# Kernel tuning notes

Hardware: AMD Instinct MI355X
Metric: run time of the kernel (lower is better)

Reference implementation:

```python
import jax, jax.numpy as jnp
import numpy as np


def setup_inputs() -> dict:
    key = jax.random.key(0)
    ks = jax.random.split(key, 6)
    B, C, H, W, O = 8, 64, 64, 64, 64
    x = jax.random.normal(ks[0], (B, C, H, W), jnp.float32)
    wq = jax.random.normal(ks[1], (O, C), jnp.float32) * 0.1
    wk = jax.random.normal(ks[2], (O, C), jnp.float32) * 0.1
    wv = jax.random.normal(ks[3], (O, C), jnp.float32) * 0.1
    rel_w = jax.random.normal(ks[4], (O, W), jnp.float32)
    rel_h = jax.random.normal(ks[5], (O, H), jnp.float32)
    return {"x": x, "wq": wq, "wk": wk, "wv": wv,
            "rel_w": rel_w, "rel_h": rel_h,
            "kernel_size": 7, "padding": 3}


def reference(x, wq, wk, wv, rel_w, rel_h, kernel_size, padding):
    B, C, H, W = x.shape
    k, p = kernel_size, padding
    # 1x1 convs (no bias) == channel matmuls
    q = jnp.einsum('bchw,oc->bohw', x, wq)                      # [B,O,H,W]
    xp = jnp.pad(x, ((0, 0), (0, 0), (p, p), (p, p)))
    k_out = jnp.einsum('bchw,oc->bohw', xp, wk)                 # [B,O,H+2p,W+2p]
    v_out = jnp.einsum('bchw,oc->bohw', xp, wv)

    def patches(t):  # torch unfold(2).unfold(3) order: row offset slowest
        return jnp.stack([t[:, :, i:i + H, j:j + W]
                          for i in range(k) for j in range(k)], axis=-1)  # [B,O,H,W,k*k]

    kp = patches(k_out)
    vp = patches(v_out)
    # relative position logits (broadcast elementwise einsums)
    rel = q * rel_w[None, :, None, :] + q * rel_h[None, :, :, None]  # [B,O,H,W]
    logits = q[..., None] * kp + rel[..., None]                 # [B,O,H,W,k*k]
    attn = jax.nn.softmax(logits, axis=-1)
    return jnp.sum(attn * vp, axis=-1)                          # [B,O,H,W]
```

## Files before the change

### kernel.cpp

```cpp
#include <hip/hip_runtime.h>
#include <hip/hip_bf16.h>

#define HW 4096

__device__ float g_qkv[3 * 8 * 64 * HW];

__global__ __launch_bounds__(256) void qkv_proj(
    const float* __restrict__ x,
    const float* __restrict__ wq,
    const float* __restrict__ wk,
    const float* __restrict__ wv)
{
    __shared__ float xs[64][64];
    const int t = threadIdx.x;
    const int b = blockIdx.x >> 6;
    const int h = blockIdx.x & 63;

    const float* xrow = x + (size_t)b * 64 * HW + (size_t)h * 64;
    for (int i = t; i < 64 * 64; i += 256) {
        int c = i >> 6, w = i & 63;
        xs[c][w] = xrow[(size_t)c * HW + w];
    }
    __syncthreads();

    const int w = t & 63;
    const int ou = __builtin_amdgcn_readfirstlane(t >> 6);

    float xr[64];
    #pragma unroll
    for (int c = 0; c < 64; ++c) xr[c] = xs[c][w];

    const float* __restrict__ mats[3] = { wq, wk, wv };
    #pragma unroll
    for (int m = 0; m < 3; ++m) {
        const float* __restrict__ wg = mats[m];
        float* op = g_qkv + ((size_t)m * 8 + b) * (64 * HW) + (size_t)h * 64 + w;
        #pragma unroll
        for (int oi = 0; oi < 16; ++oi) {
            const int o = oi * 4 + ou;
            const float* __restrict__ wrow = wg + (o << 6);
            float acc = 0.f;
            #pragma unroll
            for (int c = 0; c < 64; ++c)
                acc = fmaf(wrow[c], xr[c], acc);
            op[(size_t)o * HW] = acc;
        }
    }
}

__global__ __launch_bounds__(256) void attn(float* __restrict__ out)
{
    __shared__ float kv[70][72][2];
    const int t = threadIdx.x;
    const int b = blockIdx.x >> 6;
    const int o = blockIdx.x & 63;

    const float* qb = g_qkv + ((size_t)(0 * 8 + b) * 64 + o) * HW;
    const float* kb = g_qkv + ((size_t)(1 * 8 + b) * 64 + o) * HW;
    const float* vb = g_qkv + ((size_t)(2 * 8 + b) * 64 + o) * HW;

    for (int i = t; i < 70 * 70; i += 256) {
        int r = i / 70, c = i - r * 70;
        int gh = r - 3, gw = c - 3;
        float kk = 0.f, vv = 0.f;
        if ((unsigned)gh < 64u && (unsigned)gw < 64u) {
            kk = kb[gh * 64 + gw];
            vv = vb[gh * 64 + gw];
        }
        kv[r][c][0] = kk;
        kv[r][c][1] = vv;
    }
    __syncthreads();

    const int w = t & 63;
    const int band = t >> 6;
    #pragma unroll 1
    for (int pass = 0; pass < 2; ++pass) {
        const int hbase = band * 16 + pass * 8;
        float qv[8], den[8], num[8];
        #pragma unroll
        for (int q = 0; q < 8; ++q) {
            qv[q] = qb[(hbase + q) * 64 + w];
            den[q] = 0.f; num[q] = 0.f;
        }
        #pragma unroll
        for (int rr = 0; rr < 14; ++rr) {
            #pragma unroll
            for (int dj = 0; dj < 7; ++dj) {
                const float2 kvp = *(const float2*)&kv[hbase + rr][w + dj][0];
                #pragma unroll
                for (int q = 0; q < 8; ++q) {
                    if (rr - q >= 0 && rr - q < 7) {
                        float e = __expf(qv[q] * kvp.x);
                        den[q] += e;
                        num[q] = fmaf(e, kvp.y, num[q]);
                    }
                }
            }
        }
        #pragma unroll
        for (int q = 0; q < 8; ++q)
            out[((size_t)(b * 64 + o)) * HW + (hbase + q) * 64 + w] = num[q] / den[q];
    }
}

extern "C" void kernel_launch(void* const* d_in, const int* in_sizes, int n_in,
                              void* d_out, int out_size, void* d_ws, size_t ws_size,
                              hipStream_t stream)
{
    qkv_proj<<<dim3(512), dim3(256), 0, stream>>>(
        (const float*)d_in[0], (const float*)d_in[1],
        (const float*)d_in[2], (const float*)d_in[3]);
    attn<<<dim3(512), dim3(256), 0, stream>>>((float*)d_out);
}
```

Before: 145.7 us.

## Restructure projection accumulation and split K/V shared planes in attention

The projection kernel no longer preloads all 64 channel values into registers. It streams 4 channels at a time from shared memory and keeps 16 output accumulators, which lowers register pressure. The attention kernel stores K and V in separate shared-memory planes instead of interleaved float2 pairs, and each pass now covers 4 output rows instead of 8 (4 passes instead of 2). This cuts live registers but increases K/V row re-reads from shared memory (10 rows per 4 outputs versus 14 per 8).

```diff
diff --git a/kernel.cpp b/kernel.cpp
--- a/kernel.cpp
+++ b/kernel.cpp
@@ -26,31 +26,36 @@
     const int w = t & 63;
     const int ou = __builtin_amdgcn_readfirstlane(t >> 6);
 
-    float xr[64];
-    #pragma unroll
-    for (int c = 0; c < 64; ++c) xr[c] = xs[c][w];
-
     const float* __restrict__ mats[3] = { wq, wk, wv };
-    #pragma unroll
+    #pragma unroll 1
     for (int m = 0; m < 3; ++m) {
         const float* __restrict__ wg = mats[m];
+        float acc[16];
+        #pragma unroll
+        for (int oi = 0; oi < 16; ++oi) acc[oi] = 0.f;
+
+        #pragma unroll 2
+        for (int cb = 0; cb < 16; ++cb) {
+            float x0 = xs[cb * 4 + 0][w];
+            float x1 = xs[cb * 4 + 1][w];
+            float x2 = xs[cb * 4 + 2][w];
+            float x3 = xs[cb * 4 + 3][w];
+            #pragma unroll
+            for (int oi = 0; oi < 16; ++oi) {
+                const float* wr = wg + ((oi * 4 + ou) << 6) + cb * 4;
+                acc[oi] = fmaf(wr[3], x3, fmaf(wr[2], x2, fmaf(wr[1], x1, fmaf(wr[0], x0, acc[oi]))));
+            }
+        }
         float* op = g_qkv + ((size_t)m * 8 + b) * (64 * HW) + (size_t)h * 64 + w;
         #pragma unroll
-        for (int oi = 0; oi < 16; ++oi) {
-            const int o = oi * 4 + ou;
-            const float* __restrict__ wrow = wg + (o << 6);
-            float acc = 0.f;
-            #pragma unroll
-            for (int c = 0; c < 64; ++c)
-                acc = fmaf(wrow[c], xr[c], acc);
-            op[(size_t)o * HW] = acc;
-        }
+        for (int oi = 0; oi < 16; ++oi)
+            op[(size_t)(oi * 4 + ou) * HW] = acc[oi];
     }
 }
 
 __global__ __launch_bounds__(256) void attn(float* __restrict__ out)
 {
-    __shared__ float kv[70][72][2];
+    __shared__ float kv[70][140];
     const int t = threadIdx.x;
     const int b = blockIdx.x >> 6;
     const int o = blockIdx.x & 63;
@@ -67,40 +72,43 @@
             kk = kb[gh * 64 + gw];
             vv = vb[gh * 64 + gw];
         }
-        kv[r][c][0] = kk;
-        kv[r][c][1] = vv;
+        kv[r][c] = kk;
+        kv[r][70 + c] = vv;
     }
     __syncthreads();
 
     const int w = t & 63;
     const int band = t >> 6;
+    float* ob = out + ((size_t)(b * 64 + o)) * HW;
+
     #pragma unroll 1
-    for (int pass = 0; pass < 2; ++pass) {
-        const int hbase = band * 16 + pass * 8;
-        float qv[8], den[8], num[8];
+    for (int pass = 0; pass < 4; ++pass) {
+        const int r0 = pass * 16 + band * 4;
+        float qv[4], den[4], num[4];
         #pragma unroll
-        for (int q = 0; q < 8; ++q) {
-            qv[q] = qb[(hbase + q) * 64 + w];
-            den[q] = 0.f; num[q] = 0.f;
+        for (int j = 0; j < 4; ++j) {
+            qv[j] = qb[(r0 + j) * 64 + w];
+            den[j] = 0.f; num[j] = 0.f;
         }
         #pragma unroll
-        for (int rr = 0; rr < 14; ++rr) {
+        for (int rr = 0; rr < 10; ++rr) {
             #pragma unroll
             for (int dj = 0; dj < 7; ++dj) {
-                const float2 kvp = *(const float2*)&kv[hbase + rr][w + dj][0];
+                float kk = kv[r0 + rr][w + dj];
+                float vv = kv[r0 + rr][70 + w + dj];
                 #pragma unroll
-                for (int q = 0; q < 8; ++q) {
-                    if (rr - q >= 0 && rr - q < 7) {
-                        float e = __expf(qv[q] * kvp.x);
-                        den[q] += e;
-                        num[q] = fmaf(e, kvp.y, num[q]);
+                for (int j = 0; j < 4; ++j) {
+                    if (rr - j >= 0 && rr - j < 7) {
+                        float e = __expf(qv[j] * kk);
+                        den[j] += e;
+                        num[j] = fmaf(e, vv, num[j]);
                     }
                 }
             }
         }
         #pragma unroll
-        for (int q = 0; q < 8; ++q)
-            out[((size_t)(b * 64 + o)) * HW + (hbase + q) * 64 + w] = num[q] / den[q];
+        for (int j = 0; j < 4; ++j)
+            ob[(r0 + j) * 64 + w] = num[j] / den[j];
     }
 }
 
```

After: 155.7 us. +6.9%, slower.
